# Optimization experiments

Measured on AMD Instinct MI355X. Metric: run time of the kernel, lower is better.

The kernel has to match this reference:

```python
import jax, jax.numpy as jnp
import numpy as np

# uniform-size batching: B graphs, NC compound atoms, NP pocket residues each
B, NC, NP, H = 16, 64, 384, 128
CFEAT, PFEAT = 56, 1280
SCALE = 5.0  # coordinate_scale
LN_EPS = 1e-5


def setup_inputs() -> dict:
    key = jax.random.key(0)
    ks = jax.random.split(key, 16)
    inp = {
        "compound_feats": jax.random.normal(ks[0], (B * NC, CFEAT), jnp.float32),
        "pocket_feats": jax.random.normal(ks[1], (B * NP, PFEAT), jnp.float32),
        "complex_coords": jax.random.normal(ks[2], (B, 2 + NC + NP, 3), jnp.float32) * 10.0,
        "pocket_xyz": jax.random.normal(ks[3], (B, NP, 3), jnp.float32) * 10.0,
        "dis_map": jax.random.uniform(ks[4], (B * NP * NC,), jnp.float32) * 10.0,
        # learned parameters (xavier with gain=0.001 as in the torch init)
        "Wc": jax.random.normal(ks[5], (CFEAT, H), jnp.float32) * 0.001,
        "bc": jnp.zeros((H,), jnp.float32),
        "Wp": jax.random.normal(ks[6], (PFEAT, H), jnp.float32) * 0.001,
        "bp": jnp.zeros((H,), jnp.float32),
        "ln_g": jnp.ones((H,), jnp.float32),
        "ln_b": jnp.zeros((H,), jnp.float32),
        "W1": jax.random.normal(ks[7], (H, H), jnp.float32) * 0.001,
        "b1": jnp.zeros((H,), jnp.float32),
        "W2": jax.random.normal(ks[8], (H, 1), jnp.float32) * 0.001,
        "b2": jnp.zeros((1,), jnp.float32),
    }
    return inp


def _layernorm(x, g, b):
    m = jnp.mean(x, axis=-1, keepdims=True)
    v = jnp.mean(jnp.square(x - m), axis=-1, keepdims=True)
    return (x - m) * jax.lax.rsqrt(v + LN_EPS) * g + b


def reference(compound_feats, pocket_feats, complex_coords, pocket_xyz, dis_map,
              Wc, bc, Wp, bp, ln_g, ln_b, W1, b1, W2, b2):
    norm = lambda x: x / SCALE
    # input linears, then dense-batch (uniform sizes -> exact reshape)
    comp_emb = (compound_feats @ Wc + bc).reshape(B, NC, H)   # [B,NC,H]
    pock_emb = (pocket_feats @ Wp + bp).reshape(B, NP, H)     # [B,NP,H]
    # complex layout per graph: [glb_c, compound (NC), glb_p, pocket (NP)]
    # complex_binding_model treated as identity (see notes): emb/coords pass through.
    comp_coords_out = norm(complex_coords[:, 1:1 + NC])       # [B,NC,3] (normalized)
    pock_coords = norm(pocket_xyz)                            # [B,NP,3]
    # torch.cdist(pocket, compound): [B,NP,NC]
    diff = pock_coords[:, :, None, :] - comp_coords_out[:, None, :, :]
    pc_dis = jnp.sqrt(jnp.sum(jnp.square(diff), axis=-1))
    # layernorm + pairwise outer product + distmap MLP
    p_ln = _layernorm(pock_emb, ln_g, ln_b)
    c_ln = _layernorm(comp_emb, ln_g, ln_b)
    z = jnp.einsum('bik,bjk->bijk', p_ln, c_ln)               # [B,NP,NC,H]
    h = jax.nn.relu(z @ W1 + b1)
    b_logit = (h @ W2 + b2)[..., 0]                            # [B,NP,NC]
    # uniform sizes -> all-true masks, boolean-select is a flatten
    dis_map_pred_by_pair = jax.nn.sigmoid(b_logit.reshape(-1)) * 10.0
    dis_map_pred_by_coord = jnp.clip(pc_dis.reshape(-1) * SCALE, 0.0, 10.0)
    compound_coord_pred = (comp_coords_out * SCALE).reshape(B * NC, 3)
    compound_batch = jnp.repeat(jnp.arange(B, dtype=jnp.int32), NC)
    return (compound_coord_pred, compound_batch, dis_map_pred_by_pair,
            dis_map_pred_by_coord, dis_map)
```

## Files before the change

### kernel.cpp

```cpp
#include <hip/hip_runtime.h>
#include <hip/hip_bf16.h>

#define BB 16
#define NC 64
#define NP 384
#define HH 128
#define CF 56
#define PFT 1280

typedef float f32x4 __attribute__((ext_vector_type(4)));
typedef __bf16 bf16x8 __attribute__((ext_vector_type(8)));
typedef unsigned short u16x8 __attribute__((ext_vector_type(8)));
typedef unsigned short u16x4 __attribute__((ext_vector_type(4)));

static __device__ __forceinline__ unsigned short f2bfu(float f){
  __bf16 h = (__bf16)f;
  return __builtin_bit_cast(unsigned short, h);
}
static __device__ __forceinline__ float bfu2f(unsigned short u){
  __bf16 h = __builtin_bit_cast(__bf16, u);
  return (float)h;
}

__global__ __launch_bounds__(256) void k_prep(
    const float* __restrict__ cf, const float* __restrict__ Wc,
    const float* __restrict__ bc, const float* __restrict__ lng,
    const float* __restrict__ lnb, const float* __restrict__ Wp,
    const float* __restrict__ W1, const float* __restrict__ cc,
    const float* __restrict__ px, const float* __restrict__ dm,
    unsigned short* __restrict__ c_ln, unsigned short* __restrict__ wpt,
    unsigned short* __restrict__ w1t,
    float* __restrict__ out1, float* __restrict__ out4, float* __restrict__ out5){
  __shared__ unsigned short t[128][72];
  __shared__ float redc[2][2], redc2[2][2];
  int bx = blockIdx.x;
  int tid = threadIdx.x;
  if (bx < 20){
    int k0 = bx*64;
    #pragma unroll
    for (int i=0;i<8;i++){
      int fi = tid + i*256;
      int k  = fi>>5;
      int c4 = (fi&31)*4;
      float4 v = *(const float4*)(Wp + (size_t)(k0+k)*HH + c4);
      t[c4+0][k]=f2bfu(v.x); t[c4+1][k]=f2bfu(v.y);
      t[c4+2][k]=f2bfu(v.z); t[c4+3][k]=f2bfu(v.w);
    }
    __syncthreads();
    #pragma unroll
    for (int i=0;i<4;i++){
      int ci = tid + i*256;
      int col = ci>>3, kb = ci&7;
      u16x8 v = *(const u16x8*)&t[col][kb*8];
      *(u16x8*)(wpt + (size_t)col*PFT + k0 + kb*8) = v;
    }
  } else if (bx < 84){
    int idx = (bx-20)*256+tid;
    int k = idx>>7, m = idx&127;
    w1t[m*HH+k] = f2bfu(W1[idx]);
  } else if (bx < 596){
    int rh = tid>>7, m = tid&127;
    int row = (bx-84)*2 + rh;
    const float* cr = cf + row*CF;
    float acc = bc[m];
    #pragma unroll
    for (int k=0;k<CF;k++) acc += cr[k]*Wc[k*HH+m];
    float s=acc, s2=acc*acc;
    #pragma unroll
    for (int off=1; off<64; off<<=1){ s += __shfl_xor(s,off,64); s2 += __shfl_xor(s2,off,64); }
    int wid = (tid>>6)&1;
    if ((m&63)==0){ redc[rh][wid]=s; redc2[rh][wid]=s2; }
    __syncthreads();
    float S=redc[rh][0]+redc[rh][1], S2=redc2[rh][0]+redc2[rh][1];
    float mean = S*(1.0f/HH);
    float var  = S2*(1.0f/HH) - mean*mean;
    float rs = rsqrtf(var + 1e-5f);
    c_ln[(size_t)row*HH+m] = f2bfu((acc-mean)*rs*lng[m] + lnb[m]);
  } else if (bx < 608){
    int idx = (bx-596)*256+tid;
    if (idx < BB*NC*3){
      int bb = idx/(NC*3), rem = idx%(NC*3);
      float v = cc[(size_t)bb*(2+NC+NP)*3 + 3 + rem];
      out1[idx] = (v/5.0f)*5.0f;
    }
    if (idx < BB*NC) out1[BB*NC*3+idx] = (float)(idx>>6);
  } else {
    int idx = (bx-608)*256+tid;
    int b = idx/(NP*NC), r = idx%(NP*NC), i = r>>6, j = r&63;
    const float* pp = px + ((size_t)b*NP+i)*3;
    const float* cp = cc + (size_t)b*(2+NC+NP)*3 + 3 + (size_t)j*3;
    float dx=pp[0]/5.0f-cp[0]/5.0f;
    float dy=pp[1]/5.0f-cp[1]/5.0f;
    float dz=pp[2]/5.0f-cp[2]/5.0f;
    float d = sqrtf(dx*dx+dy*dy+dz*dz)*5.0f;
    d = fminf(fmaxf(d,0.f),10.f);
    out4[idx]=d;
    out5[idx]=dm[idx];
  }
}

__global__ __launch_bounds__(256) void k_main(
    const float* __restrict__ pf, const unsigned short* __restrict__ wpt,
    const float* __restrict__ bp, const float* __restrict__ lng,
    const float* __restrict__ lnb,
    const unsigned short* __restrict__ c_ln, const unsigned short* __restrict__ w1t,
    const float* __restrict__ b1, const float* __restrict__ W2,
    const float* __restrict__ b2p, float* __restrict__ out3){
  __shared__ __align__(16) unsigned short sA[2][16*64];
  __shared__ __align__(16) unsigned short sB[2][HH*64];
  __shared__ __align__(16) float sPf[12*HH];
  int tid = threadIdx.x;
  int w = tid>>6, lane = tid&63, q = lane&15, gr = lane>>4;
  int bx = blockIdx.x;
  int b  = bx>>5;
  int i0 = (bx&31)*12;
  size_t prow0 = (size_t)(b*NP + i0);
  *(unsigned short*)((char*)&sA[0][0] + 1536 + tid*2) = 0;
  *(unsigned short*)((char*)&sA[1][0] + 1536 + tid*2) = 0;
  f32x4 acc2[2];
  acc2[0]=(f32x4){0.f,0.f,0.f,0.f}; acc2[1]=(f32x4){0.f,0.f,0.f,0.f};
  int arow = tid>>4, ak4 = (tid&15)*4;
  float4 ra; u16x8 rb[4];
  #define LOADS1(KS) {                                                         \
    int kbase = (KS)*64;                                                       \
    if (arow < 12)                                                             \
      ra = *(const float4*)(pf + (prow0+arow)*PFT + kbase + ak4);              \
    _Pragma("unroll")                                                          \
    for (int i=0;i<4;i++){                                                     \
      int bi = tid + 256*i;                                                    \
      int col = bi>>3, kb = bi&7;                                              \
      rb[i] = *(const u16x8*)(wpt + (size_t)col*PFT + kbase + kb*8);           \
    }                                                                          \
  }
  #define WRITES1(BUF) {                                                       \
    char* A = (char*)&sA[BUF][0];                                              \
    char* Bc = (char*)&sB[BUF][0];                                             \
    if (arow < 12){                                                            \
      u16x4 h = { f2bfu(ra.x), f2bfu(ra.y), f2bfu(ra.z), f2bfu(ra.w) };        \
      *(u16x4*)(A + arow*128 + (((ak4>>3)^(arow&7))<<4) + ((ak4&7)<<1)) = h;   \
    }                                                                          \
    _Pragma("unroll")                                                          \
    for (int i=0;i<4;i++){                                                     \
      int bi = tid + 256*i;                                                    \
      int col = bi>>3, kb = bi&7;                                              \
      *(u16x8*)(Bc + col*128 + ((kb^(col&7))<<4)) = rb[i];                     \
    }                                                                          \
  }
  LOADS1(0)
  WRITES1(0)
  int cur = 0;
  for (int ks=0; ks<20; ks++){
    if (ks<19) LOADS1(ks+1)
    __syncthreads();
    char* A = (char*)&sA[cur][0];
    char* Bc = (char*)&sB[cur][0];
    #pragma unroll
    for (int kk=0;kk<2;kk++){
      bf16x8 a = *(bf16x8*)(A + q*128 + (((kk*4+gr)^(q&7))<<4));
      #pragma unroll
      for (int ct=0;ct<2;ct++){
        int col = w*32 + ct*16 + q;
        bf16x8 bfr = *(bf16x8*)(Bc + col*128 + (((kk*4+gr)^(col&7))<<4));
        acc2[ct] = __builtin_amdgcn_mfma_f32_16x16x32_bf16(a,bfr,acc2[ct],0,0,0);
      }
    }
    if (ks<19){ WRITES1(cur^1) cur ^= 1; }
  }
  __syncthreads();
  unsigned short* sW = &sB[0][0];
  #pragma unroll
  for (int ct=0;ct<2;ct++){
    int col = w*32 + ct*16 + q;
    float bpv = bp[col];
    #pragma unroll
    for (int r=0;r<4;r++){
      int row = gr*4+r;
      if (row < 12) sPf[row*HH + col] = acc2[ct][r] + bpv;
    }
  }
  {
    const int4* srcW = (const int4*)w1t;
    #pragma unroll
    for (int i=0;i<8;i++){
      int c = tid + 256*i;
      int mm = c>>4, kb = c&15;
      ((int4*)sW)[mm*16 + (kb^(mm&7))] = srcW[c];
    }
  }
  float cfr[4][8];
  {
    const unsigned short* cb = c_ln + (size_t)b*NC*HH + (size_t)(w*16+q)*HH + gr*8;
    #pragma unroll
    for (int kt=0;kt<4;kt++){
      u16x8 v = *(const u16x8*)(cb + kt*32);
      #pragma unroll
      for (int e=0;e<8;e++) cfr[kt][e] = bfu2f(v[e]);
    }
  }
  float b1v[8], w2v[8];
  #pragma unroll
  for (int nt=0;nt<8;nt++){ b1v[nt]=b1[nt*16+q]; w2v[nt]=W2[nt*16+q]; }
  float b2 = b2p[0];
  __syncthreads();
  {
    float g0 = lng[lane], g1 = lng[lane+64];
    float B0 = lnb[lane], B1 = lnb[lane+64];
    #pragma unroll
    for (int rr=0; rr<3; rr++){
      int row = w*3+rr;
      float a0 = sPf[row*HH + lane], a1 = sPf[row*HH + lane + 64];
      float s = a0+a1, s2 = a0*a0 + a1*a1;
      #pragma unroll
      for (int off=1; off<64; off<<=1){ s += __shfl_xor(s,off,64); s2 += __shfl_xor(s2,off,64); }
      float mean = s*(1.0f/HH);
      float var  = s2*(1.0f/HH) - mean*mean;
      float rs   = rsqrtf(var + 1e-5f);
      sPf[row*HH + lane]      = (a0-mean)*rs*g0 + B0;
      sPf[row*HH + lane + 64] = (a1-mean)*rs*g1 + B1;
    }
  }
  __syncthreads();
  for (int ii=0; ii<12; ii++){
    f32x4 acc[8];
    #pragma unroll
    for (int nt=0;nt<8;nt++) acc[nt]=(f32x4){0.f,0.f,0.f,0.f};
    #pragma unroll
    for (int kt=0;kt<4;kt++){
      int kblk = kt*4+gr;
      f32x4 p0 = *(const f32x4*)&sPf[ii*HH + kblk*8];
      f32x4 p1 = *(const f32x4*)&sPf[ii*HH + kblk*8 + 4];
      bf16x8 a;
      #pragma unroll
      for (int e=0;e<4;e++) a[e]   = (__bf16)(cfr[kt][e]*p0[e]);
      #pragma unroll
      for (int e=0;e<4;e++) a[e+4] = (__bf16)(cfr[kt][e+4]*p1[e]);
      #pragma unroll
      for (int nt=0;nt<8;nt++){
        int mm = nt*16+q;
        bf16x8 bv = *(const bf16x8*)&sW[mm*HH + ((kblk^(mm&7))<<3)];
        acc[nt] = __builtin_amdgcn_mfma_f32_16x16x32_bf16(a, bv, acc[nt], 0,0,0);
      }
    }
    float part[4]={0.f,0.f,0.f,0.f};
    #pragma unroll
    for (int nt=0;nt<8;nt++)
      #pragma unroll
      for (int r=0;r<4;r++){
        float h = acc[nt][r] + b1v[nt];
        h = fmaxf(h, 0.f);
        part[r] += h*w2v[nt];
      }
    #pragma unroll
    for (int r=0;r<4;r++){
      part[r]+=__shfl_xor(part[r],1,16);
      part[r]+=__shfl_xor(part[r],2,16);
      part[r]+=__shfl_xor(part[r],4,16);
      part[r]+=__shfl_xor(part[r],8,16);
    }
    if (q==0){
      float4 o;
      o.x = 10.f/(1.f+expf(-(part[0]+b2)));
      o.y = 10.f/(1.f+expf(-(part[1]+b2)));
      o.z = 10.f/(1.f+expf(-(part[2]+b2)));
      o.w = 10.f/(1.f+expf(-(part[3]+b2)));
      *(float4*)(out3 + (prow0+ii)*NC + w*16 + gr*4) = o;
    }
  }
}

extern "C" void kernel_launch(void* const* d_in, const int* in_sizes, int n_in,
                              void* d_out, int out_size, void* d_ws, size_t ws_size,
                              hipStream_t stream){
  const float* cf = (const float*)d_in[0];
  const float* pf = (const float*)d_in[1];
  const float* cc = (const float*)d_in[2];
  const float* px = (const float*)d_in[3];
  const float* dm = (const float*)d_in[4];
  const float* Wc = (const float*)d_in[5];
  const float* bc = (const float*)d_in[6];
  const float* Wp = (const float*)d_in[7];
  const float* bp = (const float*)d_in[8];
  const float* lng= (const float*)d_in[9];
  const float* lnb= (const float*)d_in[10];
  const float* W1 = (const float*)d_in[11];
  const float* b1 = (const float*)d_in[12];
  const float* W2 = (const float*)d_in[13];
  const float* b2 = (const float*)d_in[14];

  float* out = (float*)d_out;
  char* ws = (char*)d_ws;
  unsigned short* c_ln = (unsigned short*)ws;
  unsigned short* w1t  = (unsigned short*)(ws + 262144 + 1572864);
  unsigned short* wpt  = (unsigned short*)(ws + 262144 + 1572864 + 32768);

  float* out1 = out;
  float* out3 = out + BB*NC*3 + BB*NC;
  float* out4 = out3 + BB*NP*NC;
  float* out5 = out4 + BB*NP*NC;

  hipLaunchKernelGGL(k_prep, dim3(2144), dim3(256), 0, stream,
                     cf, Wc, bc, lng, lnb, Wp, W1, cc, px, dm,
                     c_ln, wpt, w1t, out1, out4, out5);
  hipLaunchKernelGGL(k_main, dim3(512), dim3(256), 0, stream,
                     pf, wpt, bp, lng, lnb, c_ln, w1t, b1, W2, b2, out3);
}
```

Before: 42.06 us.

## Split hidden dim across waves and keep W1 fragments in registers

The pair-MLP work is repartitioned so each wave handles 32 compound columns and half of the hidden dimension, instead of 16 columns and all 128 hidden units. W1 fragments are loaded once from global memory into registers rather than staged through swizzled LDS and re-read every iteration. The compound LN fragments are kept as packed bf16 and converted on the fly. Partial logits from the two hidden halves are combined through shared memory with an extra barrier before the sigmoid. The trade is higher register pressure and an extra reduction pass in exchange for removing the per-iteration LDS reads of W1.

```diff
diff --git a/kernel.cpp b/kernel.cpp
--- a/kernel.cpp
+++ b/kernel.cpp
@@ -167,7 +167,6 @@
     if (ks<19){ WRITES1(cur^1) cur ^= 1; }
   }
   __syncthreads();
-  unsigned short* sW = &sB[0][0];
   #pragma unroll
   for (int ct=0;ct<2;ct++){
     int col = w*32 + ct*16 + q;
@@ -178,29 +177,26 @@
       if (row < 12) sPf[row*HH + col] = acc2[ct][r] + bpv;
     }
   }
-  {
-    const int4* srcW = (const int4*)w1t;
-    #pragma unroll
-    for (int i=0;i<8;i++){
-      int c = tid + 256*i;
-      int mm = c>>4, kb = c&15;
-      ((int4*)sW)[mm*16 + (kb^(mm&7))] = srcW[c];
-    }
-  }
-  float cfr[4][8];
-  {
-    const unsigned short* cb = c_ln + (size_t)b*NC*HH + (size_t)(w*16+q)*HH + gr*8;
-    #pragma unroll
-    for (int kt=0;kt<4;kt++){
-      u16x8 v = *(const u16x8*)(cb + kt*32);
-      #pragma unroll
-      for (int e=0;e<8;e++) cfr[kt][e] = bfu2f(v[e]);
-    }
-  }
-  float b1v[8], w2v[8];
+  int jh = w&1, mh = w>>1;
+  int j0 = jh*32, m0 = mh*64;
+  u16x8 cfrag[2][4];
   #pragma unroll
-  for (int nt=0;nt<8;nt++){ b1v[nt]=b1[nt*16+q]; w2v[nt]=W2[nt*16+q]; }
+  for (int jt=0;jt<2;jt++){
+    const unsigned short* cb = c_ln + ((size_t)b*NC + j0 + jt*16 + q)*HH + gr*8;
+    #pragma unroll
+    for (int kt=0;kt<4;kt++) cfrag[jt][kt] = *(const u16x8*)(cb + kt*32);
+  }
+  u16x8 w1f[4][4];
+  #pragma unroll
+  for (int kt=0;kt<4;kt++)
+    #pragma unroll
+    for (int nt=0;nt<4;nt++)
+      w1f[kt][nt] = *(const u16x8*)(w1t + (size_t)(m0+nt*16+q)*HH + kt*32 + gr*8);
+  float b1v[4], w2v[4];
+  #pragma unroll
+  for (int nt=0;nt<4;nt++){ b1v[nt]=b1[m0+nt*16+q]; w2v[nt]=W2[m0+nt*16+q]; }
   float b2 = b2p[0];
+  float* psumh = (float*)&sB[0][0];
   __syncthreads();
   {
     float g0 = lng[lane], g1 = lng[lane+64];
@@ -221,50 +217,60 @@
   }
   __syncthreads();
   for (int ii=0; ii<12; ii++){
-    f32x4 acc[8];
-    #pragma unroll
-    for (int nt=0;nt<8;nt++) acc[nt]=(f32x4){0.f,0.f,0.f,0.f};
+    f32x4 acc[2][4];
+    #pragma unroll
+    for (int jt=0;jt<2;jt++)
+      #pragma unroll
+      for (int nt=0;nt<4;nt++) acc[jt][nt]=(f32x4){0.f,0.f,0.f,0.f};
     #pragma unroll
     for (int kt=0;kt<4;kt++){
       int kblk = kt*4+gr;
       f32x4 p0 = *(const f32x4*)&sPf[ii*HH + kblk*8];
       f32x4 p1 = *(const f32x4*)&sPf[ii*HH + kblk*8 + 4];
-      bf16x8 a;
-      #pragma unroll
-      for (int e=0;e<4;e++) a[e]   = (__bf16)(cfr[kt][e]*p0[e]);
-      #pragma unroll
-      for (int e=0;e<4;e++) a[e+4] = (__bf16)(cfr[kt][e+4]*p1[e]);
-      #pragma unroll
-      for (int nt=0;nt<8;nt++){
-        int mm = nt*16+q;
-        bf16x8 bv = *(const bf16x8*)&sW[mm*HH + ((kblk^(mm&7))<<3)];
-        acc[nt] = __builtin_amdgcn_mfma_f32_16x16x32_bf16(a, bv, acc[nt], 0,0,0);
+      #pragma unroll
+      for (int jt=0;jt<2;jt++){
+        u16x8 cfv = cfrag[jt][kt];
+        bf16x8 a;
+        #pragma unroll
+        for (int e=0;e<4;e++) a[e]   = (__bf16)(bfu2f(cfv[e])*p0[e]);
+        #pragma unroll
+        for (int e=0;e<4;e++) a[e+4] = (__bf16)(bfu2f(cfv[e+4])*p1[e]);
+        #pragma unroll
+        for (int nt=0;nt<4;nt++)
+          acc[jt][nt] = __builtin_amdgcn_mfma_f32_16x16x32_bf16(
+              a, __builtin_bit_cast(bf16x8, w1f[kt][nt]), acc[jt][nt], 0,0,0);
       }
     }
-    float part[4]={0.f,0.f,0.f,0.f};
-    #pragma unroll
-    for (int nt=0;nt<8;nt++)
+    #pragma unroll
+    for (int jt=0;jt<2;jt++){
+      float part[4]={0.f,0.f,0.f,0.f};
+      #pragma unroll
+      for (int nt=0;nt<4;nt++)
+        #pragma unroll
+        for (int r=0;r<4;r++){
+          float h = acc[jt][nt][r] + b1v[nt];
+          h = fmaxf(h, 0.f);
+          part[r] += h*w2v[nt];
+        }
       #pragma unroll
       for (int r=0;r<4;r++){
-        float h = acc[nt][r] + b1v[nt];
-        h = fmaxf(h, 0.f);
-        part[r] += h*w2v[nt];
+        part[r]+=__shfl_xor(part[r],1,16);
+        part[r]+=__shfl_xor(part[r],2,16);
+        part[r]+=__shfl_xor(part[r],4,16);
+        part[r]+=__shfl_xor(part[r],8,16);
       }
-    #pragma unroll
-    for (int r=0;r<4;r++){
-      part[r]+=__shfl_xor(part[r],1,16);
-      part[r]+=__shfl_xor(part[r],2,16);
-      part[r]+=__shfl_xor(part[r],4,16);
-      part[r]+=__shfl_xor(part[r],8,16);
-    }
-    if (q==0){
-      float4 o;
-      o.x = 10.f/(1.f+expf(-(part[0]+b2)));
-      o.y = 10.f/(1.f+expf(-(part[1]+b2)));
-      o.z = 10.f/(1.f+expf(-(part[2]+b2)));
-      o.w = 10.f/(1.f+expf(-(part[3]+b2)));
-      *(float4*)(out3 + (prow0+ii)*NC + w*16 + gr*4) = o;
-    }
+      if (q==0){
+        #pragma unroll
+        for (int r=0;r<4;r++)
+          psumh[(mh*12 + ii)*64 + j0 + jt*16 + gr*4 + r] = part[r];
+      }
+    }
+  }
+  __syncthreads();
+  for (int v=tid; v<12*64; v+=256){
+    int ii = v>>6, j = v&63;
+    float s = psumh[(0*12+ii)*64 + j] + psumh[(1*12+ii)*64 + j] + b2;
+    out3[(prow0+ii)*NC + j] = 10.f/(1.f+expf(-s));
   }
 }
 
```

Result: slower. 45.45 us (+8.0%).
